# Optimization experiments

Measured on AMD Instinct MI355X. Metric: run time of the kernel, lower is better.

## Reference

```python
import jax, jax.numpy as jnp
import numpy as np

TAU = 2.0          # LIF membrane time constant
V_TH = 1.0         # spike threshold (spikingjelly default)
BN_EPS = 1e-5

T, C_IN, C_OUT, L = 16, 512, 512, 4096


def setup_inputs() -> dict:
    key = jax.random.key(0)
    k1, k2 = jax.random.split(key)
    x = jax.random.normal(k1, (T, C_IN, L), dtype=jnp.float32)
    W = jax.random.normal(k2, (C_OUT, C_IN), dtype=jnp.float32) * 0.02
    gamma = jnp.ones((C_OUT,), dtype=jnp.float32)
    beta = jnp.zeros((C_OUT,), dtype=jnp.float32)
    return {"x": x, "W": W, "gamma": gamma, "beta": beta}


def reference(x, W, gamma, beta):
    # 1x1 Conv1d (bias=False): [T, Cin, L] x [Cout, Cin] -> [T, Cout, L]
    y = jnp.einsum("tcl,oc->tol", x, W)

    # BatchNorm1d in training mode: normalize per channel over (T, L)
    mean = jnp.mean(y, axis=(0, 2), keepdims=True)
    var = jnp.mean(jnp.square(y - mean), axis=(0, 2), keepdims=True)  # biased var
    y = (y - mean) * jax.lax.rsqrt(var + BN_EPS)
    y = y * gamma[None, :, None] + beta[None, :, None]

    # Multi-step LIF: v' = v + (x - v)/tau ; spike = H(v' - vth) ; hard reset to 0
    def step(v, x_t):
        v = v + (x_t - v) / TAU
        s = (v >= V_TH).astype(v.dtype)
        v = v * (1.0 - s)  # v_reset = 0
        return v, s

    v0 = jnp.zeros_like(y[0])
    _, spikes = jax.lax.scan(step, v0, y)
    return spikes
```

## Files before the change

kernel.cpp:

```cpp
#include <hip/hip_runtime.h>


#define T_STEPS 16
#define CIN 512
#define COUT 512
#define LDIM 4096
#define KB 32
#define NL (COUT * LDIM)

typedef float v2f __attribute__((ext_vector_type(2)));

static constexpr size_t NY = (size_t)T_STEPS * NL;

__device__ float g_yf[NY];
__device__ float g_mr[2 * COUT];
__device__ int   g_bf16;

__device__ __forceinline__ float b2f(unsigned short u) {
    return __uint_as_float(((unsigned int)u) << 16);
}
__device__ __forceinline__ float blo(unsigned int u) {
    return __uint_as_float(u << 16);
}
__device__ __forceinline__ float bhi(unsigned int u) {
    return __uint_as_float(u & 0xFFFF0000u);
}

__global__ void detect_dtype(const unsigned int* __restrict__ gamma_words) {
    if (threadIdx.x == 0)
        g_bf16 = (gamma_words[0] == 0x3F803F80u) ? 1 : 0;
}

__global__ __launch_bounds__(256) void gemm_np(
    const void* __restrict__ xin, const void* __restrict__ win,
    float* __restrict__ yws, int use_ws)
{
#pragma clang fp contract(off)
    float* __restrict__ y = use_ws ? yws : g_yf;
    const int bf = g_bf16;

    __shared__ float Ws[KB][64];
    __shared__ float Xs[KB][128];

    const int lb = blockIdx.x * 128;
    const int ob = blockIdx.y * 64;
    const int t  = blockIdx.z;

    const int tid = threadIdx.x;
    const int tx = tid & 15;
    const int ty = tid >> 4;

    const int wrow = tid >> 2;
    const int wk   = (tid & 3) * 8;
    const int xk   = tid >> 3;
    const int xl   = (tid & 7) * 16;

    const size_t wbase = (size_t)(ob + wrow) * CIN + wk;
    const size_t xbase = (size_t)t * CIN * LDIM + (size_t)xk * LDIM + lb + xl;

    v2f acc[4][4];
    #pragma unroll
    for (int i = 0; i < 4; i++)
        #pragma unroll
        for (int j = 0; j < 4; j++) acc[i][j] = (v2f)(0.0f);

    for (int k0 = 0; k0 < CIN; k0 += KB) {
        float wv[8], xv[16];
        if (bf) {
            uint4 wu = *reinterpret_cast<const uint4*>(
                (const unsigned short*)win + wbase + k0);
            uint4 xu0 = *reinterpret_cast<const uint4*>(
                (const unsigned short*)xin + xbase + (size_t)k0 * LDIM);
            uint4 xu1 = *reinterpret_cast<const uint4*>(
                (const unsigned short*)xin + xbase + (size_t)k0 * LDIM + 8);
            wv[0]=blo(wu.x); wv[1]=bhi(wu.x); wv[2]=blo(wu.y); wv[3]=bhi(wu.y);
            wv[4]=blo(wu.z); wv[5]=bhi(wu.z); wv[6]=blo(wu.w); wv[7]=bhi(wu.w);
            xv[0]=blo(xu0.x); xv[1]=bhi(xu0.x); xv[2]=blo(xu0.y); xv[3]=bhi(xu0.y);
            xv[4]=blo(xu0.z); xv[5]=bhi(xu0.z); xv[6]=blo(xu0.w); xv[7]=bhi(xu0.w);
            xv[8]=blo(xu1.x); xv[9]=bhi(xu1.x); xv[10]=blo(xu1.y); xv[11]=bhi(xu1.y);
            xv[12]=blo(xu1.z); xv[13]=bhi(xu1.z); xv[14]=blo(xu1.w); xv[15]=bhi(xu1.w);
        } else {
            float4 w0 = *reinterpret_cast<const float4*>((const float*)win + wbase + k0);
            float4 w1 = *reinterpret_cast<const float4*>((const float*)win + wbase + k0 + 4);
            wv[0]=w0.x; wv[1]=w0.y; wv[2]=w0.z; wv[3]=w0.w;
            wv[4]=w1.x; wv[5]=w1.y; wv[6]=w1.z; wv[7]=w1.w;
            #pragma unroll
            for (int m = 0; m < 4; m++) {
                float4 xf = *reinterpret_cast<const float4*>(
                    (const float*)xin + xbase + (size_t)k0 * LDIM + m * 4);
                xv[m*4+0]=xf.x; xv[m*4+1]=xf.y; xv[m*4+2]=xf.z; xv[m*4+3]=xf.w;
            }
        }
        __syncthreads();
        #pragma unroll
        for (int m = 0; m < 8; m++) Ws[wk + m][wrow] = wv[m];
        #pragma unroll
        for (int m = 0; m < 4; m++) {
            float4 st = {xv[m*4+0], xv[m*4+1], xv[m*4+2], xv[m*4+3]};
            *reinterpret_cast<float4*>(&Xs[xk][xl + m * 4]) = st;
        }
        __syncthreads();

        #pragma unroll
        for (int kk = 0; kk < KB; ++kk) {
            const float4 w4 = *reinterpret_cast<const float4*>(&Ws[kk][ty * 4]);
            const float4 xa = *reinterpret_cast<const float4*>(&Xs[kk][tx * 8]);
            const float4 xb = *reinterpret_cast<const float4*>(&Xs[kk][tx * 8 + 4]);
            v2f xp[4];
            xp[0] = (v2f){xa.x, xa.y}; xp[1] = (v2f){xa.z, xa.w};
            xp[2] = (v2f){xb.x, xb.y}; xp[3] = (v2f){xb.z, xb.w};
            const float wr[4] = {w4.x, w4.y, w4.z, w4.w};
            #pragma unroll
            for (int i = 0; i < 4; i++) {
                v2f wp = (v2f){wr[i], wr[i]};
                #pragma unroll
                for (int j = 0; j < 4; j++) {
                    v2f p = wp * xp[j];
                    acc[i][j] = acc[i][j] + p;
                }
            }
        }
    }

    #pragma unroll
    for (int i = 0; i < 4; i++) {
        size_t row = (size_t)t * COUT + ob + ty * 4 + i;
        float* yp = &y[row * LDIM + lb + tx * 8];
        float4 s0 = {acc[i][0].x, acc[i][0].y, acc[i][1].x, acc[i][1].y};
        float4 s1 = {acc[i][2].x, acc[i][2].y, acc[i][3].x, acc[i][3].y};
        *reinterpret_cast<float4*>(yp) = s0;
        *reinterpret_cast<float4*>(yp + 4) = s1;
    }
}

__global__ __launch_bounds__(256) void bn_stats_np(
    const float* __restrict__ yws, int use_ws)
{
#pragma clang fp contract(off)
    const float* __restrict__ y = use_ws ? yws : g_yf;
    const int o = blockIdx.x;
    const int g = threadIdx.x >> 3;
    const int l = threadIdx.x & 7;

    __shared__ float leaves[32];
    __shared__ float mean_sh;
    __shared__ float acc_sh[2];

    for (int phase = 0; phase < 2; ++phase) {
        __syncthreads();
        const float mean = (phase == 1) ? mean_sh : 0.0f;
        for (int t = 0; t < T_STEPS; ++t) {
            const float* row = &y[(size_t)t * NL + (size_t)o * LDIM + g * 128];
            float r[8];
            #pragma unroll
            for (int q = 0; q < 8; q++) {
                float a = row[q * 8 + l];
                float b = row[64 + q * 8 + l];
                if (phase == 1) {
                    float da = a - mean; a = da * da;
                    float db = b - mean; b = db * db;
                }
                r[q] = a + b;
            }
            float s01 = r[0] + r[1], s23 = r[2] + r[3];
            float s45 = r[4] + r[5], s67 = r[6] + r[7];
            float S = (s01 + s23) + (s45 + s67);
            S = S + __shfl_xor(S, 1);
            S = S + __shfl_xor(S, 2);
            S = S + __shfl_xor(S, 4);
            __syncthreads();
            if (l == 0) leaves[g] = S;
            __syncthreads();
            if (threadIdx.x == 0) {
                float a16[16], a8[8], a4[4], a2[2];
                #pragma unroll
                for (int k = 0; k < 16; k++) a16[k] = leaves[2*k] + leaves[2*k+1];
                #pragma unroll
                for (int k = 0; k < 8;  k++) a8[k] = a16[2*k] + a16[2*k+1];
                #pragma unroll
                for (int k = 0; k < 4;  k++) a4[k] = a8[2*k] + a8[2*k+1];
                #pragma unroll
                for (int k = 0; k < 2;  k++) a2[k] = a4[2*k] + a4[2*k+1];
                float pw = a2[0] + a2[1];
                if (t == 0) acc_sh[phase] = pw;
                else        acc_sh[phase] = acc_sh[phase] + pw;
            }
            __syncthreads();
        }
        if (threadIdx.x == 0) {
            if (phase == 0) {
                mean_sh = __fdiv_rn(acc_sh[0], 65536.0f);
            } else {
                float var = __fdiv_rn(acc_sh[1], 65536.0f);
                float rr = __fdiv_rn(1.0f, __fsqrt_rn(var + 1e-5f));
                g_mr[o] = mean_sh;
                g_mr[COUT + o] = rr;
            }
        }
    }
}

__global__ __launch_bounds__(256) void lif_np(
    const void* __restrict__ gin, const void* __restrict__ bin,
    void* __restrict__ outv, const float* __restrict__ yws, int use_ws)
{
#pragma clang fp contract(off)
    const float* __restrict__ y = use_ws ? yws : g_yf;
    const int bf = g_bf16;
    const int idx = blockIdx.x * 256 + threadIdx.x;
    const int o = idx >> 12;
    const float mean = g_mr[o];
    const float r    = g_mr[COUT + o];
    float gm, bt;
    if (bf) {
        gm = b2f(((const unsigned short*)gin)[o]);
        bt = b2f(((const unsigned short*)bin)[o]);
    } else {
        gm = ((const float*)gin)[o];
        bt = ((const float*)bin)[o];
    }
    float v = 0.0f;
    #pragma unroll
    for (int t = 0; t < T_STEPS; t++) {
        float yv = y[(size_t)t * NL + idx];
        float d  = yv - mean;
        float n1 = d * r;
        float n2 = n1 * gm;
        float n3 = n2 + bt;
        float dv = n3 - v;
        float h  = dv * 0.5f;
        v = v + h;
        float s;
        if (v >= 1.0f) { s = 1.0f; v = 0.0f; } else { s = 0.0f; }
        if (bf) ((unsigned short*)outv)[(size_t)t * NL + idx] = (s == 1.0f) ? 0x3F80 : 0x0000;
        else    ((float*)outv)[(size_t)t * NL + idx] = s;
    }
}

extern "C" void kernel_launch(void* const* d_in, const int* in_sizes, int n_in,
                              void* d_out, int out_size, void* d_ws, size_t ws_size,
                              hipStream_t stream) {
    const void* x     = d_in[0];
    const void* W     = d_in[1];
    const void* gamma = d_in[2];
    const void* beta  = d_in[3];

    const int use_ws = (ws_size >= NY * sizeof(float)) ? 1 : 0;
    float* yws = (float*)d_ws;

    detect_dtype<<<1, 64, 0, stream>>>((const unsigned int*)gamma);

    dim3 grid(LDIM / 128, COUT / 64, T_STEPS);
    gemm_np<<<grid, 256, 0, stream>>>(x, W, yws, use_ws);

    bn_stats_np<<<COUT, 256, 0, stream>>>(yws, use_ws);

    lif_np<<<NL / 256, 256, 0, stream>>>(gamma, beta, d_out, yws, use_ws);
}
```

Measured before the change: 885.2 us.

## Enlarge GEMM tile to 128x256 with 8x8 register blocking and packed-FMA asm

The conv GEMM tile grows from 64x128 to 128x256 outputs per block, so each thread accumulates an 8x8 block of float pairs. Shared arrays are padded to cut bank conflicts, and global loads are issued before the barrier so they overlap the previous compute. Inline v_pk_mul_f32 with op_sel broadcasts a weight lane, which removes the separate broadcast moves. The cost is much higher register pressure, fewer blocks per CU, and exact mul-then-add rounding still kept.

```diff
diff --git a/kernel.cpp b/kernel.cpp
--- a/kernel.cpp
+++ b/kernel.cpp
@@ -6,6 +6,8 @@
 #define COUT 512
 #define LDIM 4096
 #define KB 32
+#define WPAD 132
+#define XPAD 260
 #define NL (COUT * LDIM)
 
 typedef float v2f __attribute__((ext_vector_type(2)));
@@ -26,12 +28,30 @@
     return __uint_as_float(u & 0xFFFF0000u);
 }
 
+__device__ __forceinline__ v2f pk_mul_lo(v2f w, v2f x) {
+    v2f d;
+    asm("v_pk_mul_f32 %0, %1, %2 op_sel:[0,0] op_sel_hi:[0,1]"
+        : "=v"(d) : "v"(w), "v"(x));
+    return d;
+}
+__device__ __forceinline__ v2f pk_mul_hi(v2f w, v2f x) {
+    v2f d;
+    asm("v_pk_mul_f32 %0, %1, %2 op_sel:[1,0] op_sel_hi:[1,1]"
+        : "=v"(d) : "v"(w), "v"(x));
+    return d;
+}
+__device__ __forceinline__ v2f pk_add(v2f a, v2f b) {
+    v2f d;
+    asm("v_pk_add_f32 %0, %1, %2" : "=v"(d) : "v"(a), "v"(b));
+    return d;
+}
+
 __global__ void detect_dtype(const unsigned int* __restrict__ gamma_words) {
     if (threadIdx.x == 0)
         g_bf16 = (gamma_words[0] == 0x3F803F80u) ? 1 : 0;
 }
 
-__global__ __launch_bounds__(256) void gemm_np(
+__global__ __launch_bounds__(256, 2) void gemm_np(
     const void* __restrict__ xin, const void* __restrict__ win,
     float* __restrict__ yws, int use_ws)
 {
@@ -39,97 +59,125 @@
     float* __restrict__ y = use_ws ? yws : g_yf;
     const int bf = g_bf16;
 
-    __shared__ float Ws[KB][64];
-    __shared__ float Xs[KB][128];
-
-    const int lb = blockIdx.x * 128;
-    const int ob = blockIdx.y * 64;
+    __shared__ float Ws[KB][WPAD];
+    __shared__ float Xs[KB][XPAD];
+
+    const int lb = blockIdx.x * 256;
+    const int ob = blockIdx.y * 128;
     const int t  = blockIdx.z;
 
     const int tid = threadIdx.x;
     const int tx = tid & 15;
     const int ty = tid >> 4;
 
-    const int wrow = tid >> 2;
-    const int wk   = (tid & 3) * 8;
-    const int xk   = tid >> 3;
-    const int xl   = (tid & 7) * 16;
-
-    const size_t wbase = (size_t)(ob + wrow) * CIN + wk;
-    const size_t xbase = (size_t)t * CIN * LDIM + (size_t)xk * LDIM + lb + xl;
-
-    v2f acc[4][4];
+    const int wo = tid >> 1;
+    const int wh = tid & 1;
+    const int xk = tid >> 3;
+    const int xo = tid & 7;
+
+    const size_t wrowbase = (size_t)(ob + wo) * CIN + wh * 16;
+    const size_t xrowbase = (size_t)t * CIN * LDIM + (size_t)xk * LDIM + lb;
+
+    v2f acc[8][8];
     #pragma unroll
-    for (int i = 0; i < 4; i++)
+    for (int i = 0; i < 8; i++)
         #pragma unroll
-        for (int j = 0; j < 4; j++) acc[i][j] = (v2f)(0.0f);
+        for (int j = 0; j < 8; j++) acc[i][j] = (v2f)(0.0f);
 
     for (int k0 = 0; k0 < CIN; k0 += KB) {
-        float wv[8], xv[16];
         if (bf) {
-            uint4 wu = *reinterpret_cast<const uint4*>(
-                (const unsigned short*)win + wbase + k0);
-            uint4 xu0 = *reinterpret_cast<const uint4*>(
-                (const unsigned short*)xin + xbase + (size_t)k0 * LDIM);
-            uint4 xu1 = *reinterpret_cast<const uint4*>(
-                (const unsigned short*)xin + xbase + (size_t)k0 * LDIM + 8);
-            wv[0]=blo(wu.x); wv[1]=bhi(wu.x); wv[2]=blo(wu.y); wv[3]=bhi(wu.y);
-            wv[4]=blo(wu.z); wv[5]=bhi(wu.z); wv[6]=blo(wu.w); wv[7]=bhi(wu.w);
-            xv[0]=blo(xu0.x); xv[1]=bhi(xu0.x); xv[2]=blo(xu0.y); xv[3]=bhi(xu0.y);
-            xv[4]=blo(xu0.z); xv[5]=bhi(xu0.z); xv[6]=blo(xu0.w); xv[7]=bhi(xu0.w);
-            xv[8]=blo(xu1.x); xv[9]=bhi(xu1.x); xv[10]=blo(xu1.y); xv[11]=bhi(xu1.y);
-            xv[12]=blo(xu1.z); xv[13]=bhi(xu1.z); xv[14]=blo(xu1.w); xv[15]=bhi(xu1.w);
+            uint4 wa[2], xa[4];
+            const unsigned short* wp = (const unsigned short*)win + wrowbase + k0;
+            const unsigned short* xp8 = (const unsigned short*)xin + xrowbase +
+                                        (size_t)k0 * LDIM + xo * 8;
+            #pragma unroll
+            for (int m = 0; m < 2; m++)
+                wa[m] = *reinterpret_cast<const uint4*>(wp + m * 8);
+            #pragma unroll
+            for (int m = 0; m < 4; m++)
+                xa[m] = *reinterpret_cast<const uint4*>(xp8 + m * 64);
+            __syncthreads();
+            #pragma unroll
+            for (int m = 0; m < 2; m++) {
+                const unsigned int uu[4] = {wa[m].x, wa[m].y, wa[m].z, wa[m].w};
+                #pragma unroll
+                for (int e = 0; e < 4; e++) {
+                    Ws[wh * 16 + m * 8 + e * 2 + 0][wo] = blo(uu[e]);
+                    Ws[wh * 16 + m * 8 + e * 2 + 1][wo] = bhi(uu[e]);
+                }
+            }
+            #pragma unroll
+            for (int m = 0; m < 4; m++) {
+                const unsigned int uu[4] = {xa[m].x, xa[m].y, xa[m].z, xa[m].w};
+                float4 f0 = {blo(uu[0]), bhi(uu[0]), blo(uu[1]), bhi(uu[1])};
+                float4 f1 = {blo(uu[2]), bhi(uu[2]), blo(uu[3]), bhi(uu[3])};
+                *reinterpret_cast<float4*>(&Xs[xk][xo * 8 + m * 64 + 0]) = f0;
+                *reinterpret_cast<float4*>(&Xs[xk][xo * 8 + m * 64 + 4]) = f1;
+            }
         } else {
-            float4 w0 = *reinterpret_cast<const float4*>((const float*)win + wbase + k0);
-            float4 w1 = *reinterpret_cast<const float4*>((const float*)win + wbase + k0 + 4);
-            wv[0]=w0.x; wv[1]=w0.y; wv[2]=w0.z; wv[3]=w0.w;
-            wv[4]=w1.x; wv[5]=w1.y; wv[6]=w1.z; wv[7]=w1.w;
+            float4 wf[4], xf[8];
+            const float* wp = (const float*)win + wrowbase + k0;
+            const float* xp4 = (const float*)xin + xrowbase + (size_t)k0 * LDIM + xo * 4;
+            #pragma unroll
+            for (int m = 0; m < 4; m++)
+                wf[m] = *reinterpret_cast<const float4*>(wp + m * 4);
+            #pragma unroll
+            for (int m = 0; m < 8; m++)
+                xf[m] = *reinterpret_cast<const float4*>(xp4 + m * 32);
+            __syncthreads();
             #pragma unroll
             for (int m = 0; m < 4; m++) {
-                float4 xf = *reinterpret_cast<const float4*>(
-                    (const float*)xin + xbase + (size_t)k0 * LDIM + m * 4);
-                xv[m*4+0]=xf.x; xv[m*4+1]=xf.y; xv[m*4+2]=xf.z; xv[m*4+3]=xf.w;
-            }
+                Ws[wh * 16 + m * 4 + 0][wo] = wf[m].x;
+                Ws[wh * 16 + m * 4 + 1][wo] = wf[m].y;
+                Ws[wh * 16 + m * 4 + 2][wo] = wf[m].z;
+                Ws[wh * 16 + m * 4 + 3][wo] = wf[m].w;
+            }
+            #pragma unroll
+            for (int m = 0; m < 8; m++)
+                *reinterpret_cast<float4*>(&Xs[xk][xo * 4 + m * 32]) = xf[m];
         }
         __syncthreads();
-        #pragma unroll
-        for (int m = 0; m < 8; m++) Ws[wk + m][wrow] = wv[m];
+
+        #pragma unroll 8
+        for (int kk = 0; kk < KB; ++kk) {
+            const float4 wA = *reinterpret_cast<const float4*>(&Ws[kk][ty * 4]);
+            const float4 wB = *reinterpret_cast<const float4*>(&Ws[kk][64 + ty * 4]);
+            v2f wp4[4];
+            wp4[0] = (v2f){wA.x, wA.y}; wp4[1] = (v2f){wA.z, wA.w};
+            wp4[2] = (v2f){wB.x, wB.y}; wp4[3] = (v2f){wB.z, wB.w};
+            v2f xp[8];
+            #pragma unroll
+            for (int m = 0; m < 4; m++) {
+                const float4 xv = *reinterpret_cast<const float4*>(&Xs[kk][tx * 4 + m * 64]);
+                xp[2 * m + 0] = (v2f){xv.x, xv.y};
+                xp[2 * m + 1] = (v2f){xv.z, xv.w};
+            }
+            #pragma unroll
+            for (int io = 0; io < 8; io++) {
+                const v2f w = wp4[io >> 1];
+                if (io & 1) {
+                    #pragma unroll
+                    for (int j = 0; j < 8; j++)
+                        acc[io][j] = pk_add(acc[io][j], pk_mul_hi(w, xp[j]));
+                } else {
+                    #pragma unroll
+                    for (int j = 0; j < 8; j++)
+                        acc[io][j] = pk_add(acc[io][j], pk_mul_lo(w, xp[j]));
+                }
+            }
+        }
+    }
+
+    #pragma unroll
+    for (int io = 0; io < 8; io++) {
+        const int o = ob + (io >> 2) * 64 + ty * 4 + (io & 3);
+        float* yp = &y[((size_t)t * COUT + o) * LDIM + lb + tx * 4];
         #pragma unroll
         for (int m = 0; m < 4; m++) {
-            float4 st = {xv[m*4+0], xv[m*4+1], xv[m*4+2], xv[m*4+3]};
-            *reinterpret_cast<float4*>(&Xs[xk][xl + m * 4]) = st;
-        }
-        __syncthreads();
-
-        #pragma unroll
-        for (int kk = 0; kk < KB; ++kk) {
-            const float4 w4 = *reinterpret_cast<const float4*>(&Ws[kk][ty * 4]);
-            const float4 xa = *reinterpret_cast<const float4*>(&Xs[kk][tx * 8]);
-            const float4 xb = *reinterpret_cast<const float4*>(&Xs[kk][tx * 8 + 4]);
-            v2f xp[4];
-            xp[0] = (v2f){xa.x, xa.y}; xp[1] = (v2f){xa.z, xa.w};
-            xp[2] = (v2f){xb.x, xb.y}; xp[3] = (v2f){xb.z, xb.w};
-            const float wr[4] = {w4.x, w4.y, w4.z, w4.w};
-            #pragma unroll
-            for (int i = 0; i < 4; i++) {
-                v2f wp = (v2f){wr[i], wr[i]};
-                #pragma unroll
-                for (int j = 0; j < 4; j++) {
-                    v2f p = wp * xp[j];
-                    acc[i][j] = acc[i][j] + p;
-                }
-            }
-        }
-    }
-
-    #pragma unroll
-    for (int i = 0; i < 4; i++) {
-        size_t row = (size_t)t * COUT + ob + ty * 4 + i;
-        float* yp = &y[row * LDIM + lb + tx * 8];
-        float4 s0 = {acc[i][0].x, acc[i][0].y, acc[i][1].x, acc[i][1].y};
-        float4 s1 = {acc[i][2].x, acc[i][2].y, acc[i][3].x, acc[i][3].y};
-        *reinterpret_cast<float4*>(yp) = s0;
-        *reinterpret_cast<float4*>(yp + 4) = s1;
+            float4 s = {acc[io][2 * m].x, acc[io][2 * m].y,
+                        acc[io][2 * m + 1].x, acc[io][2 * m + 1].y};
+            *reinterpret_cast<float4*>(yp + m * 64) = s;
+        }
     }
 }
 
@@ -250,7 +298,7 @@
 
     detect_dtype<<<1, 64, 0, stream>>>((const unsigned int*)gamma);
 
-    dim3 grid(LDIM / 128, COUT / 64, T_STEPS);
+    dim3 grid(LDIM / 256, COUT / 128, T_STEPS);
     gemm_np<<<grid, 256, 0, stream>>>(x, W, yws, use_ws);
 
     bn_stats_np<<<COUT, 256, 0, stream>>>(yws, use_ws);
```

After: 874.0 us. No clear change (-1.3%).
